# Optimization experiments

Hardware: AMD Instinct MI355X
Metric: run time of the kernel (lower is better)

## Reference

```python
import jax, jax.numpy as jnp
import numpy as np
import math

N = 8192
IN_FEATURES = 512
OUT_FEATURES = 64
NEG_INF = -9e15

def setup_inputs() -> dict:
    key = jax.random.key(0)
    k1, k2, k3, k4 = jax.random.split(key, 4)
    inp = jax.random.normal(k1, (N, IN_FEATURES), dtype=jnp.float32)
    adj = jax.random.randint(k2, (N, N), 0, 2, dtype=jnp.int32)
    # xavier_uniform with gain=1.414 for [in, out] weights
    limit = 1.414 * math.sqrt(6.0 / (IN_FEATURES + OUT_FEATURES))
    kW = jax.random.uniform(k3, (IN_FEATURES, OUT_FEATURES), dtype=jnp.float32, minval=-limit, maxval=limit)
    vW = jax.random.uniform(k4, (IN_FEATURES, OUT_FEATURES), dtype=jnp.float32, minval=-limit, maxval=limit)
    return {"input": inp, "adj": adj, "kW": kW, "vW": vW}

def reference(input, adj, kW, vW):
    kh = input @ kW                      # [N, d]
    vh = input @ vW                      # [N, d]
    d = kh.shape[1]
    K = (kh @ kh.T) / jnp.sqrt(jnp.asarray(d, dtype=kh.dtype))  # [N, N]
    scores = jnp.where(adj > 0, K, jnp.asarray(NEG_INF, dtype=K.dtype))
    attention = jax.nn.softmax(scores, axis=1)
    # dropout is a no-op (p=0.0 / eval mode)
    h_prime = attention @ vh             # [N, d]
    return jax.nn.elu(h_prime)           # concat=True path
```

## Files before the change

kernel.cpp:

```cpp
#include <hip/hip_runtime.h>
#include <math.h>

typedef __bf16 bf16_t;
typedef __bf16 bf16x8 __attribute__((ext_vector_type(8)));
typedef float f32x4 __attribute__((ext_vector_type(4)));

#define NN 8192
#define L2E 1.44269504088896340736f
#define SMAX 45.0f
#define KSCALE 0.35355339059327373f

__global__ __launch_bounds__(256) void prep_kernel(
    const float* __restrict__ input,
    const float* __restrict__ kW,
    const float* __restrict__ vW,
    const int*   __restrict__ adj,
    bf16_t* __restrict__ inputH,
    bf16_t* __restrict__ inputL,
    bf16_t* __restrict__ wimgH,
    bf16_t* __restrict__ wimgL,
    unsigned int* __restrict__ bits)
{
    const int b = blockIdx.x;
    if (b < 2048) {
        const size_t idx = ((size_t)b * 256 + threadIdx.x) * 8;
        f32x4 a0 = *(const f32x4*)&input[idx];
        f32x4 a1 = *(const f32x4*)&input[idx + 4];
        bf16x8 h8, l8;
        #pragma unroll
        for (int j = 0; j < 4; ++j) {
            bf16_t h0 = (bf16_t)a0[j], h1 = (bf16_t)a1[j];
            h8[j]     = h0;  l8[j]     = (bf16_t)(a0[j] - (float)h0);
            h8[4 + j] = h1;  l8[4 + j] = (bf16_t)(a1[j] - (float)h1);
        }
        *(bf16x8*)&inputH[idx] = h8;
        *(bf16x8*)&inputL[idx] = l8;
    } else if (b < 2080) {
        const int gid  = (b - 2048) * 256 + threadIdx.x;
        const int proj = gid >> 12;
        const int r    = gid & 4095;
        const int frag = r >> 6;
        const int lane = r & 63;
        const int kc   = frag >> 2;
        const int nb   = frag & 3;
        const int quad = lane >> 4;
        const int l15  = lane & 15;
        const float* W = proj ? vW : kW;
        bf16x8 h8, l8;
        #pragma unroll
        for (int j = 0; j < 8; ++j) {
            float w  = W[(size_t)(kc * 32 + quad * 8 + j) * 64 + nb * 16 + l15];
            bf16_t h = (bf16_t)w;
            h8[j] = h;
            l8[j] = (bf16_t)(w - (float)h);
        }
        ((bf16x8*)wimgH)[gid] = h8;
        ((bf16x8*)wimgL)[gid] = l8;
    } else {
        const int lane = threadIdx.x & 63;
        const int gw   = (b - 2080) * 4 + (threadIdx.x >> 6);
        const int nw   = 2048 * 4;
        const int nchunks = (NN / 256) * NN;
        for (int c = gw; c < nchunks; c += nw) {
            const int* p = adj + (size_t)c * 256;
            unsigned int* o = bits + (size_t)c * 8;
            #pragma unroll
            for (int k = 0; k < 4; ++k) {
                int v = p[k * 64 + lane];
                unsigned long long m = __ballot(v > 0);
                if (lane == 0) *(uint2*)(o + 2 * k) = *(uint2*)&m;
            }
        }
    }
}

__global__ __launch_bounds__(512) void proj_kernel(
    const bf16_t* __restrict__ inputH,
    const bf16_t* __restrict__ inputL,
    const bf16_t* __restrict__ wimgH,
    const bf16_t* __restrict__ wimgL,
    bf16_t* __restrict__ khs_hi,
    bf16_t* __restrict__ khs_lo,
    bf16_t* __restrict__ khsF,
    bf16_t* __restrict__ vhF)
{
    const int tid   = threadIdx.x;
    const int w     = tid >> 6;
    const int lane  = tid & 63;
    const int proj  = w >> 2;
    const int nb    = w & 3;
    const int l15   = lane & 15;
    const int quad  = lane >> 4;
    const int rbase = blockIdx.x * 16;

    const bf16x8* ah_p = (const bf16x8*)&inputH[(size_t)(rbase + l15) * 512 + quad * 8];
    const bf16x8* al_p = (const bf16x8*)&inputL[(size_t)(rbase + l15) * 512 + quad * 8];
    const bf16x8* bh_p = (const bf16x8*)wimgH + ((size_t)proj * 64 + nb) * 64 + lane;
    const bf16x8* bl_p = (const bf16x8*)wimgL + ((size_t)proj * 64 + nb) * 64 + lane;

    f32x4 acc = {};
    #pragma unroll
    for (int kc = 0; kc < 16; ++kc) {
        bf16x8 ah = ah_p[kc * 4];
        bf16x8 al = al_p[kc * 4];
        bf16x8 bh = bh_p[(size_t)kc * 256];
        bf16x8 bl = bl_p[(size_t)kc * 256];
        acc = __builtin_amdgcn_mfma_f32_16x16x32_bf16(ah, bh, acc, 0, 0, 0);
        acc = __builtin_amdgcn_mfma_f32_16x16x32_bf16(al, bh, acc, 0, 0, 0);
        acc = __builtin_amdgcn_mfma_f32_16x16x32_bf16(ah, bl, acc, 0, 0, 0);
    }

    const int dcol = nb * 16 + l15;
    if (proj == 0) {
        const int kcF = nb >> 1;
        const int lf  = (quad * 4) + ((((nb << 1) + (l15 >> 3)) & 3) << 4);
        const int jF  = l15 & 7;
        bf16_t* kf = &khsF[((size_t)(blockIdx.x * 2 + kcF) * 64 + lf) * 8 + jF];
        #pragma unroll
        for (int r = 0; r < 4; ++r) {
            float v  = acc[r] * KSCALE;
            bf16_t h = (bf16_t)v;
            khs_hi[(size_t)(rbase + quad * 4 + r) * 64 + dcol] = h;
            khs_lo[(size_t)(rbase + quad * 4 + r) * 64 + dcol] = (bf16_t)(v - (float)h);
            kf[r * 8] = h;
        }
    } else {
        const int kt = blockIdx.x >> 1;
        const int lf = l15 + ((((blockIdx.x << 1) + (quad >> 1)) & 3) << 4);
        union { bf16_t b[4]; uint2 u; } pk;
        #pragma unroll
        for (int r = 0; r < 4; ++r) pk.b[r] = (bf16_t)acc[r];
        *(uint2*)&vhF[((size_t)(kt * 4 + nb) * 64 + lf) * 8 + (quad & 1) * 4] = pk.u;
    }
}

__global__ __launch_bounds__(512, 4) void attn_kernel(
    const unsigned int* __restrict__ bits,
    const bf16_t* __restrict__ khs_hi,
    const bf16_t* __restrict__ khs_lo,
    const bf16_t* __restrict__ khsF,
    const bf16_t* __restrict__ vhF,
    float* __restrict__ out)
{
    __shared__ __align__(16) float M[4 * 16 * 68];

    const int tid   = threadIdx.x;
    const int w     = tid >> 6;
    const int lane  = tid & 63;
    const int l15   = lane & 15;
    const int quad  = lane >> 4;
    const int qbase = blockIdx.x * 16;
    const int colstart = w * 1024;

    const bf16x8 qh0 = *(const bf16x8*)&khs_hi[(size_t)(qbase + l15) * 64 + quad * 8];
    const bf16x8 qh1 = *(const bf16x8*)&khs_hi[(size_t)(qbase + l15) * 64 + 32 + quad * 8];
    const bf16x8 ql0 = *(const bf16x8*)&khs_lo[(size_t)(qbase + l15) * 64 + quad * 8];
    const bf16x8 ql1 = *(const bf16x8*)&khs_lo[(size_t)(qbase + l15) * 64 + 32 + quad * 8];

    bf16x8 ones;
    #pragma unroll
    for (int j = 0; j < 8; ++j) ones[j] = (bf16_t)1.0f;

    f32x4 o0 = {}, o1 = {}, o2 = {}, o3 = {}, o4 = {};

    const unsigned int* bpl = bits + (size_t)(qbase + l15) * 256 + (colstart >> 5);
    unsigned int mcur = bpl[0], mnxt;

    const bf16x8* kF = (const bf16x8*)khsF + (size_t)(colstart >> 4) * 128 + lane;
    const bf16x8* vF = (const bf16x8*)vhF  + (size_t)(colstart >> 5) * 256 + lane;

    const int idxA = (l15 + (((2 * quad)    ) & 3) * 16) * 4;
    const int idxB = (l15 + (((2 * quad) | 1) & 3) * 16) * 4;

    for (int t = 0; t < 32; ++t) {
        bf16x8 bh00 = kF[t * 256];
        bf16x8 bh01 = kF[t * 256 + 64];
        bf16x8 bh10 = kF[t * 256 + 128];
        bf16x8 bh11 = kF[t * 256 + 192];
        bf16x8 bv0  = vF[t * 256];
        bf16x8 bv1  = vF[t * 256 + 64];
        bf16x8 bv2  = vF[t * 256 + 128];
        bf16x8 bv3  = vF[t * 256 + 192];

        mnxt = bpl[(t + 1) & 31];

        f32x4 zz = {};
        f32x4 s0 = __builtin_amdgcn_mfma_f32_16x16x32_bf16(bh00, qh0, zz, 0, 0, 0);
        s0 = __builtin_amdgcn_mfma_f32_16x16x32_bf16(bh01, qh1, s0, 0, 0, 0);
        s0 = __builtin_amdgcn_mfma_f32_16x16x32_bf16(bh00, ql0, s0, 0, 0, 0);
        s0 = __builtin_amdgcn_mfma_f32_16x16x32_bf16(bh01, ql1, s0, 0, 0, 0);
        f32x4 s1 = __builtin_amdgcn_mfma_f32_16x16x32_bf16(bh10, qh0, zz, 0, 0, 0);
        s1 = __builtin_amdgcn_mfma_f32_16x16x32_bf16(bh11, qh1, s1, 0, 0, 0);
        s1 = __builtin_amdgcn_mfma_f32_16x16x32_bf16(bh10, ql0, s1, 0, 0, 0);
        s1 = __builtin_amdgcn_mfma_f32_16x16x32_bf16(bh11, ql1, s1, 0, 0, 0);

        union { bf16_t b[2]; int u; } k0, k1, k2, k3;
        #pragma unroll
        for (int r = 0; r < 4; ++r) {
            float p0 = ((mcur >> (quad * 4 + r)) & 1u)
                         ? __builtin_amdgcn_exp2f((s0[r] - SMAX) * L2E) : 0.f;
            float p1 = ((mcur >> (16 + quad * 4 + r)) & 1u)
                         ? __builtin_amdgcn_exp2f((s1[r] - SMAX) * L2E) : 0.f;
            if (r < 2) { k0.b[r] = (bf16_t)p0; k2.b[r] = (bf16_t)p1; }
            else       { k1.b[r - 2] = (bf16_t)p0; k3.b[r - 2] = (bf16_t)p1; }
        }

        int a0 = __builtin_amdgcn_ds_bpermute(idxA, k0.u);
        int a1 = __builtin_amdgcn_ds_bpermute(idxA, k1.u);
        int a2 = __builtin_amdgcn_ds_bpermute(idxB, k0.u);
        int a3 = __builtin_amdgcn_ds_bpermute(idxB, k1.u);
        int c0 = __builtin_amdgcn_ds_bpermute(idxA, k2.u);
        int c1 = __builtin_amdgcn_ds_bpermute(idxA, k3.u);
        int c2 = __builtin_amdgcn_ds_bpermute(idxB, k2.u);
        int c3 = __builtin_amdgcn_ds_bpermute(idxB, k3.u);

        union { int u[4]; bf16x8 v; } pa;
        pa.u[0] = quad < 2 ? a0 : c0;
        pa.u[1] = quad < 2 ? a1 : c1;
        pa.u[2] = quad < 2 ? a2 : c2;
        pa.u[3] = quad < 2 ? a3 : c3;

        o0 = __builtin_amdgcn_mfma_f32_16x16x32_bf16(pa.v, bv0, o0, 0, 0, 0);
        o1 = __builtin_amdgcn_mfma_f32_16x16x32_bf16(pa.v, bv1, o1, 0, 0, 0);
        o2 = __builtin_amdgcn_mfma_f32_16x16x32_bf16(pa.v, bv2, o2, 0, 0, 0);
        o3 = __builtin_amdgcn_mfma_f32_16x16x32_bf16(pa.v, bv3, o3, 0, 0, 0);
        o4 = __builtin_amdgcn_mfma_f32_16x16x32_bf16(pa.v, ones, o4, 0, 0, 0);

        mcur = mnxt;
    }

    #pragma unroll
    for (int s = 4; s >= 1; s >>= 1) {
        __syncthreads();
        if (w >= s && w < 2 * s) {
            float* base = M + (w - s) * 16 * 68;
            #pragma unroll
            for (int r = 0; r < 4; ++r) {
                const int row = quad * 4 + r;
                base[row * 68 + l15]      = o0[r];
                base[row * 68 + 16 + l15] = o1[r];
                base[row * 68 + 32 + l15] = o2[r];
                base[row * 68 + 48 + l15] = o3[r];
                if (l15 == 0) base[row * 68 + 64] = o4[r];
            }
        }
        __syncthreads();
        if (w < s) {
            float* base = M + w * 16 * 68;
            #pragma unroll
            for (int r = 0; r < 4; ++r) {
                const int row = quad * 4 + r;
                o0[r] += base[row * 68 + l15];
                o1[r] += base[row * 68 + 16 + l15];
                o2[r] += base[row * 68 + 32 + l15];
                o3[r] += base[row * 68 + 48 + l15];
                o4[r] += base[row * 68 + 64];
            }
        }
    }

    if (w == 0) {
        #pragma unroll
        for (int r = 0; r < 4; ++r) {
            const size_t row = (size_t)qbase + quad * 4 + r;
            float l   = o4[r];
            float inv = 1.0f / (l > 0.f ? l : 1.0f);
            float v0 = o0[r] * inv, v1 = o1[r] * inv, v2 = o2[r] * inv, v3 = o3[r] * inv;
            out[row * 64 + l15]      = v0 > 0.f ? v0 : expm1f(v0);
            out[row * 64 + 16 + l15] = v1 > 0.f ? v1 : expm1f(v1);
            out[row * 64 + 32 + l15] = v2 > 0.f ? v2 : expm1f(v2);
            out[row * 64 + 48 + l15] = v3 > 0.f ? v3 : expm1f(v3);
        }
    }
}

extern "C" void kernel_launch(void* const* d_in, const int* in_sizes, int n_in,
                              void* d_out, int out_size, void* d_ws, size_t ws_size,
                              hipStream_t stream) {
    const float* input = nullptr;
    const int*   adj   = nullptr;
    const float* kW    = nullptr;
    const float* vW    = nullptr;
    for (int i = 0; i < n_in; ++i) {
        if (in_sizes[i] == 8192 * 512)            input = (const float*)d_in[i];
        else if (in_sizes[i] == 512 * 64) {
            if (!kW) kW = (const float*)d_in[i]; else vW = (const float*)d_in[i];
        } else                                    adj = (const int*)d_in[i];
    }
    float* out = (float*)d_out;

    char* ws = (char*)d_ws;
    bf16_t*       khs_hi = (bf16_t*)(ws);
    bf16_t*       khs_lo = (bf16_t*)(ws + (1u << 20));
    bf16_t*       khsF   = (bf16_t*)(ws + (2u << 20));
    bf16_t*       vhF    = (bf16_t*)(ws + (3u << 20));
    unsigned int* bits   = (unsigned int*)(ws + (4u << 20));
    bf16_t*       inputH = (bf16_t*)(ws + (12u << 20));
    bf16_t*       inputL = (bf16_t*)(ws + (20u << 20));
    bf16_t*       wimgH  = (bf16_t*)(ws + (28u << 20));
    bf16_t*       wimgL  = (bf16_t*)(ws + (28u << 20) + (128u << 10));

    prep_kernel<<<4128, 256, 0, stream>>>(input, kW, vW, adj,
                                          inputH, inputL, wimgH, wimgL, bits);
    proj_kernel<<<512, 512, 0, stream>>>(inputH, inputL, wimgH, wimgL,
                                         khs_hi, khs_lo, khsF, vhF);
    attn_kernel<<<512, 512, 0, stream>>>(bits, khs_hi, khs_lo, khsF, vhF, out);
}
```

Before: 459.6 us.

## Move adjacency bit-packing into projection kernel and prefetch next K fragments

The adjacency ballot-packing work moves out of the prep kernel and into extra blocks of the projection launch, so the memory-bound 256MB adj read can overlap with the projection MFMA work instead of running before it. Separately, the attention loop now loads the next iteration's K fragments early (software prefetch) so they arrive before they are needed. The prefetch raises register pressure, and the merged launch's block scheduling can let the pack blocks crowd out projection blocks.

```diff
diff --git a/kernel.cpp b/kernel.cpp
--- a/kernel.cpp
+++ b/kernel.cpp
@@ -10,16 +10,14 @@
 #define SMAX 45.0f
 #define KSCALE 0.35355339059327373f
 
-__global__ __launch_bounds__(256) void prep_kernel(
+__global__ __launch_bounds__(256) void prep1_kernel(
     const float* __restrict__ input,
     const float* __restrict__ kW,
     const float* __restrict__ vW,
-    const int*   __restrict__ adj,
     bf16_t* __restrict__ inputH,
     bf16_t* __restrict__ inputL,
     bf16_t* __restrict__ wimgH,
-    bf16_t* __restrict__ wimgL,
-    unsigned int* __restrict__ bits)
+    bf16_t* __restrict__ wimgL)
 {
     const int b = blockIdx.x;
     if (b < 2048) {
@@ -35,7 +33,7 @@
         }
         *(bf16x8*)&inputH[idx] = h8;
         *(bf16x8*)&inputL[idx] = l8;
-    } else if (b < 2080) {
+    } else {
         const int gid  = (b - 2048) * 256 + threadIdx.x;
         const int proj = gid >> 12;
         const int r    = gid & 4095;
@@ -56,10 +54,27 @@
         }
         ((bf16x8*)wimgH)[gid] = h8;
         ((bf16x8*)wimgL)[gid] = l8;
-    } else {
-        const int lane = threadIdx.x & 63;
-        const int gw   = (b - 2080) * 4 + (threadIdx.x >> 6);
-        const int nw   = 2048 * 4;
+    }
+}
+
+__global__ __launch_bounds__(512) void projpack_kernel(
+    const bf16_t* __restrict__ inputH,
+    const bf16_t* __restrict__ inputL,
+    const bf16_t* __restrict__ wimgH,
+    const bf16_t* __restrict__ wimgL,
+    const int*    __restrict__ adj,
+    bf16_t* __restrict__ khs_hi,
+    bf16_t* __restrict__ khs_lo,
+    bf16_t* __restrict__ khsF,
+    bf16_t* __restrict__ vhF,
+    unsigned int* __restrict__ bits)
+{
+    const int tid   = threadIdx.x;
+    const int lane  = tid & 63;
+
+    if (blockIdx.x >= 512) {
+        const int gw = (blockIdx.x - 512) * 8 + (tid >> 6);
+        const int nw = 1024 * 8;
         const int nchunks = (NN / 256) * NN;
         for (int c = gw; c < nchunks; c += nw) {
             const int* p = adj + (size_t)c * 256;
@@ -71,22 +86,10 @@
                 if (lane == 0) *(uint2*)(o + 2 * k) = *(uint2*)&m;
             }
         }
-    }
-}
-
-__global__ __launch_bounds__(512) void proj_kernel(
-    const bf16_t* __restrict__ inputH,
-    const bf16_t* __restrict__ inputL,
-    const bf16_t* __restrict__ wimgH,
-    const bf16_t* __restrict__ wimgL,
-    bf16_t* __restrict__ khs_hi,
-    bf16_t* __restrict__ khs_lo,
-    bf16_t* __restrict__ khsF,
-    bf16_t* __restrict__ vhF)
-{
-    const int tid   = threadIdx.x;
+        return;
+    }
+
     const int w     = tid >> 6;
-    const int lane  = tid & 63;
     const int proj  = w >> 2;
     const int nb    = w & 3;
     const int l15   = lane & 15;
@@ -172,15 +175,16 @@
     const int idxA = (l15 + (((2 * quad)    ) & 3) * 16) * 4;
     const int idxB = (l15 + (((2 * quad) | 1) & 3) * 16) * 4;
 
+    bf16x8 bh00 = kF[0];
+    bf16x8 bh01 = kF[64];
+    bf16x8 bh10 = kF[128];
+    bf16x8 bh11 = kF[192];
+
     for (int t = 0; t < 32; ++t) {
-        bf16x8 bh00 = kF[t * 256];
-        bf16x8 bh01 = kF[t * 256 + 64];
-        bf16x8 bh10 = kF[t * 256 + 128];
-        bf16x8 bh11 = kF[t * 256 + 192];
-        bf16x8 bv0  = vF[t * 256];
-        bf16x8 bv1  = vF[t * 256 + 64];
-        bf16x8 bv2  = vF[t * 256 + 128];
-        bf16x8 bv3  = vF[t * 256 + 192];
+        bf16x8 bv0 = vF[t * 256];
+        bf16x8 bv1 = vF[t * 256 + 64];
+        bf16x8 bv2 = vF[t * 256 + 128];
+        bf16x8 bv3 = vF[t * 256 + 192];
 
         mnxt = bpl[(t + 1) & 31];
 
@@ -194,6 +198,12 @@
         s1 = __builtin_amdgcn_mfma_f32_16x16x32_bf16(bh10, ql0, s1, 0, 0, 0);
         s1 = __builtin_amdgcn_mfma_f32_16x16x32_bf16(bh11, ql1, s1, 0, 0, 0);
 
+        const int tn = (t + 1) & 31;
+        bf16x8 nh00 = kF[tn * 256];
+        bf16x8 nh01 = kF[tn * 256 + 64];
+        bf16x8 nh10 = kF[tn * 256 + 128];
+        bf16x8 nh11 = kF[tn * 256 + 192];
+
         union { bf16_t b[2]; int u; } k0, k1, k2, k3;
         #pragma unroll
         for (int r = 0; r < 4; ++r) {
@@ -226,6 +236,7 @@
         o3 = __builtin_amdgcn_mfma_f32_16x16x32_bf16(pa.v, bv3, o3, 0, 0, 0);
         o4 = __builtin_amdgcn_mfma_f32_16x16x32_bf16(pa.v, ones, o4, 0, 0, 0);
 
+        bh00 = nh00; bh01 = nh01; bh10 = nh10; bh11 = nh11;
         mcur = mnxt;
     }
 
@@ -300,9 +311,8 @@
     bf16_t*       wimgH  = (bf16_t*)(ws + (28u << 20));
     bf16_t*       wimgL  = (bf16_t*)(ws + (28u << 20) + (128u << 10));
 
-    prep_kernel<<<4128, 256, 0, stream>>>(input, kW, vW, adj,
-                                          inputH, inputL, wimgH, wimgL, bits);
-    proj_kernel<<<512, 512, 0, stream>>>(inputH, inputL, wimgH, wimgL,
-                                         khs_hi, khs_lo, khsF, vhF);
+    prep1_kernel<<<2080, 256, 0, stream>>>(input, kW, vW, inputH, inputL, wimgH, wimgL);
+    projpack_kernel<<<1536, 512, 0, stream>>>(inputH, inputL, wimgH, wimgL, adj,
+                                              khs_hi, khs_lo, khsF, vhF, bits);
     attn_kernel<<<512, 512, 0, stream>>>(bits, khs_hi, khs_lo, khsF, vhF, out);
 }
```

Result: no change. 468.3 us (+1.9%).

## Fuse adjacency bitmask packing into attention kernel via per-wave LDS staging

Applied to the files above, without the earlier changes.

The separate pass that read the full int32 adjacency matrix and wrote a packed bitmask to global memory is removed. The attention kernel now reads adj directly, packs each 4-int vector into bits with lane shuffles, and stores the per-wave mask in shared memory. The first 256-column chunk is packed up front and later chunks are prefetched and packed inside the main loop, overlapping the load with MFMA work. This drops the bitmask write and read-back, but adds global loads, shuffles and LDS traffic to the main loop and makes it depend on LDS ordering within each wave.

```diff
diff --git a/kernel.cpp b/kernel.cpp
--- a/kernel.cpp
+++ b/kernel.cpp
@@ -4,22 +4,21 @@
 typedef __bf16 bf16_t;
 typedef __bf16 bf16x8 __attribute__((ext_vector_type(8)));
 typedef float f32x4 __attribute__((ext_vector_type(4)));
+typedef int   i32x4 __attribute__((ext_vector_type(4)));
 
 #define NN 8192
 #define L2E 1.44269504088896340736f
 #define SMAX 45.0f
 #define KSCALE 0.35355339059327373f
 
-__global__ __launch_bounds__(256) void prep_kernel(
+__global__ __launch_bounds__(256) void prep1_kernel(
     const float* __restrict__ input,
     const float* __restrict__ kW,
     const float* __restrict__ vW,
-    const int*   __restrict__ adj,
     bf16_t* __restrict__ inputH,
     bf16_t* __restrict__ inputL,
     bf16_t* __restrict__ wimgH,
-    bf16_t* __restrict__ wimgL,
-    unsigned int* __restrict__ bits)
+    bf16_t* __restrict__ wimgL)
 {
     const int b = blockIdx.x;
     if (b < 2048) {
@@ -35,7 +34,7 @@
         }
         *(bf16x8*)&inputH[idx] = h8;
         *(bf16x8*)&inputL[idx] = l8;
-    } else if (b < 2080) {
+    } else {
         const int gid  = (b - 2048) * 256 + threadIdx.x;
         const int proj = gid >> 12;
         const int r    = gid & 4095;
@@ -56,21 +55,6 @@
         }
         ((bf16x8*)wimgH)[gid] = h8;
         ((bf16x8*)wimgL)[gid] = l8;
-    } else {
-        const int lane = threadIdx.x & 63;
-        const int gw   = (b - 2080) * 4 + (threadIdx.x >> 6);
-        const int nw   = 2048 * 4;
-        const int nchunks = (NN / 256) * NN;
-        for (int c = gw; c < nchunks; c += nw) {
-            const int* p = adj + (size_t)c * 256;
-            unsigned int* o = bits + (size_t)c * 8;
-            #pragma unroll
-            for (int k = 0; k < 4; ++k) {
-                int v = p[k * 64 + lane];
-                unsigned long long m = __ballot(v > 0);
-                if (lane == 0) *(uint2*)(o + 2 * k) = *(uint2*)&m;
-            }
-        }
     }
 }
 
@@ -135,14 +119,14 @@
 }
 
 __global__ __launch_bounds__(512, 4) void attn_kernel(
-    const unsigned int* __restrict__ bits,
+    const int* __restrict__ adj,
     const bf16_t* __restrict__ khs_hi,
     const bf16_t* __restrict__ khs_lo,
     const bf16_t* __restrict__ khsF,
     const bf16_t* __restrict__ vhF,
     float* __restrict__ out)
 {
-    __shared__ __align__(16) float M[4 * 16 * 68];
+    __shared__ __align__(16) unsigned int SMEM[4352];
 
     const int tid   = threadIdx.x;
     const int w     = tid >> 6;
@@ -152,6 +136,8 @@
     const int qbase = blockIdx.x * 16;
     const int colstart = w * 1024;
 
+    unsigned int* maskW = SMEM + w * 544;
+
     const bf16x8 qh0 = *(const bf16x8*)&khs_hi[(size_t)(qbase + l15) * 64 + quad * 8];
     const bf16x8 qh1 = *(const bf16x8*)&khs_hi[(size_t)(qbase + l15) * 64 + 32 + quad * 8];
     const bf16x8 ql0 = *(const bf16x8*)&khs_lo[(size_t)(qbase + l15) * 64 + quad * 8];
@@ -163,16 +149,34 @@
 
     f32x4 o0 = {}, o1 = {}, o2 = {}, o3 = {}, o4 = {};
 
-    const unsigned int* bpl = bits + (size_t)(qbase + l15) * 256 + (colstart >> 5);
-    unsigned int mcur = bpl[0], mnxt;
-
     const bf16x8* kF = (const bf16x8*)khsF + (size_t)(colstart >> 4) * 128 + lane;
     const bf16x8* vF = (const bf16x8*)vhF  + (size_t)(colstart >> 5) * 256 + lane;
 
     const int idxA = (l15 + (((2 * quad)    ) & 3) * 16) * 4;
     const int idxB = (l15 + (((2 * quad) | 1) & 3) * 16) * 4;
 
+    const int* adjw = adj + (size_t)qbase * NN + colstart + lane * 4;
+
+    #pragma unroll 4
+    for (int r = 0; r < 16; ++r) {
+        i32x4 v = *(const i32x4*)(adjw + (size_t)r * NN);
+        int n = (v[0] > 0) | ((v[1] > 0) << 1) | ((v[2] > 0) << 2) | ((v[3] > 0) << 3);
+        n |= __shfl_xor(n, 1) << 4;
+        n |= __shfl_xor(n, 2) << 8;
+        n |= __shfl_xor(n, 4) << 16;
+        if ((lane & 7) == 0) maskW[r * 34 + (lane >> 3)] = (unsigned int)n;
+    }
+
     for (int t = 0; t < 32; ++t) {
+        i32x4 sa = {}, sb = {};
+        int sr0 = 0, sc = 0;
+        if (t < 24) {
+            sc  = (t >> 3) + 1;
+            sr0 = (t & 7) * 2;
+            sa = *(const i32x4*)(adjw + (size_t)sr0 * NN + sc * 256);
+            sb = *(const i32x4*)(adjw + (size_t)(sr0 + 1) * NN + sc * 256);
+        }
+
         bf16x8 bh00 = kF[t * 256];
         bf16x8 bh01 = kF[t * 256 + 64];
         bf16x8 bh10 = kF[t * 256 + 128];
@@ -182,7 +186,7 @@
         bf16x8 bv2  = vF[t * 256 + 128];
         bf16x8 bv3  = vF[t * 256 + 192];
 
-        mnxt = bpl[(t + 1) & 31];
+        unsigned int mcur = maskW[l15 * 34 + t];
 
         f32x4 zz = {};
         f32x4 s0 = __builtin_amdgcn_mfma_f32_16x16x32_bf16(bh00, qh0, zz, 0, 0, 0);
@@ -226,9 +230,23 @@
         o3 = __builtin_amdgcn_mfma_f32_16x16x32_bf16(pa.v, bv3, o3, 0, 0, 0);
         o4 = __builtin_amdgcn_mfma_f32_16x16x32_bf16(pa.v, ones, o4, 0, 0, 0);
 
-        mcur = mnxt;
-    }
-
+        if (t < 24) {
+            int n0 = (sa[0] > 0) | ((sa[1] > 0) << 1) | ((sa[2] > 0) << 2) | ((sa[3] > 0) << 3);
+            n0 |= __shfl_xor(n0, 1) << 4;
+            n0 |= __shfl_xor(n0, 2) << 8;
+            n0 |= __shfl_xor(n0, 4) << 16;
+            int n1 = (sb[0] > 0) | ((sb[1] > 0) << 1) | ((sb[2] > 0) << 2) | ((sb[3] > 0) << 3);
+            n1 |= __shfl_xor(n1, 1) << 4;
+            n1 |= __shfl_xor(n1, 2) << 8;
+            n1 |= __shfl_xor(n1, 4) << 16;
+            if ((lane & 7) == 0) {
+                maskW[sr0 * 34 + sc * 8 + (lane >> 3)]       = (unsigned int)n0;
+                maskW[(sr0 + 1) * 34 + sc * 8 + (lane >> 3)] = (unsigned int)n1;
+            }
+        }
+    }
+
+    float* M = (float*)SMEM;
     #pragma unroll
     for (int s = 4; s >= 1; s >>= 1) {
         __syncthreads();
@@ -294,15 +312,13 @@
     bf16_t*       khs_lo = (bf16_t*)(ws + (1u << 20));
     bf16_t*       khsF   = (bf16_t*)(ws + (2u << 20));
     bf16_t*       vhF    = (bf16_t*)(ws + (3u << 20));
-    unsigned int* bits   = (unsigned int*)(ws + (4u << 20));
     bf16_t*       inputH = (bf16_t*)(ws + (12u << 20));
     bf16_t*       inputL = (bf16_t*)(ws + (20u << 20));
     bf16_t*       wimgH  = (bf16_t*)(ws + (28u << 20));
     bf16_t*       wimgL  = (bf16_t*)(ws + (28u << 20) + (128u << 10));
 
-    prep_kernel<<<4128, 256, 0, stream>>>(input, kW, vW, adj,
-                                          inputH, inputL, wimgH, wimgL, bits);
+    prep1_kernel<<<2080, 256, 0, stream>>>(input, kW, vW, inputH, inputL, wimgH, wimgL);
     proj_kernel<<<512, 512, 0, stream>>>(inputH, inputL, wimgH, wimgL,
                                          khs_hi, khs_lo, khsF, vhF);
-    attn_kernel<<<512, 512, 0, stream>>>(bits, khs_hi, khs_lo, khsF, vhF, out);
+    attn_kernel<<<512, 512, 0, stream>>>(adj, khs_hi, khs_lo, khsF, vhF, out);
 }
```

Result: faster. 424.5 us (median of 2 runs) (-7.6%).
